# Kernel tuning notes

Measured on AMD Instinct MI355X. Metric: run time of the kernel, lower is better.

The kernel has to match this reference:

```python
import jax, jax.numpy as jnp
import numpy as np

B, S, K, N = 4, 2048, 4096, 4096

def setup_inputs() -> dict:
    key = jax.random.key(0)
    k1, k2, k3, k4 = jax.random.split(key, 4)
    # int8 quantized activations and weight (stored as int8, matmul accumulates int32)
    a = jax.random.randint(k1, (B, S, K), -128, 128, dtype=jnp.int32).astype(jnp.int8)
    w = jax.random.randint(k3, (K, N), -128, 128, dtype=jnp.int32).astype(jnp.int8)
    # dequant scales: per-token for activations, per-output-channel for weight
    a_s = (jax.random.uniform(k2, (B, S, 1), dtype=jnp.float32) + 0.5) * 0.01
    w_s = (jax.random.uniform(k4, (1, N), dtype=jnp.float32) + 0.5) * 0.01
    return {"a": a, "a_s": a_s, "w": w, "w_s": w_s}

def reference(a, a_s, w, w_s):
    # torch._int_mm loop with padding), fused with dequant epilogue.
    acc = jnp.einsum('bsk,kn->bsn', a, w, preferred_element_type=jnp.int32)
    # dequant: float32 accum * input_scale * weight_scale, cast to model dtype (fp16)
    out = (acc.astype(jnp.float32) * a_s * w_s).astype(jnp.float16)
    return out
```

## Files before the change

### kernel.cpp

```cpp
#include <hip/hip_runtime.h>
#include <cstdint>
#include <cstddef>


#define M_DIM 8192
#define N_DIM 4096
#define K_DIM 4096

#define PREP_A_BLOCKS ((M_DIM / 32) * (K_DIM / 128))
#define PREP_W_BLOCKS ((N_DIM / 64) * (K_DIM / 64))

typedef int v4i  __attribute__((ext_vector_type(4)));
typedef int v16i __attribute__((ext_vector_type(16)));

__device__ __forceinline__ uint32_t pack4(int x, int y, int z, int w)
{
    return (uint32_t)(x & 0xff) | ((uint32_t)(y & 0xff) << 8) |
           ((uint32_t)(z & 0xff) << 16) | ((uint32_t)(w & 0xff) << 24);
}

__global__ void __launch_bounds__(256) prepare_kernel(
    const int* __restrict__ a, const int* __restrict__ w,
    uint8_t* __restrict__ a_f, uint8_t* __restrict__ w_f)
{
    __shared__ int lds[64][65];
    const int t = threadIdx.x;

    if (blockIdx.x < PREP_A_BLOCKS) {
        uint32_t* l32 = (uint32_t*)&lds[0][0];
        const int bm = blockIdx.x >> 5;
        const int bk = blockIdx.x & 31;
        const int m0 = bm * 32;
        const int k0 = bk * 128;
#pragma unroll
        for (int i = 0; i < 4; ++i) {
            const int f = i * 256 + t;
            const int r = f >> 5;
            const int c = (f << 2) & 127;
            int4 x = *(const int4*)(a + (size_t)(m0 + r) * K_DIM + k0 + c);
            uint32_t u = pack4(x.x, x.y, x.z, x.w);
            const int region = c >> 5;
            const int chunk  = r + (((c >> 4) & 1) << 5);
            const int wd     = region * 256 + chunk * 4 + ((c & 15) >> 2);
            l32[wd ^ ((region & 3) << 3)] = u;
        }
        __syncthreads();
        uint4 o = ((const uint4*)l32)[t ^ (((t >> 6) & 3) << 1)];
        *(uint4*)(a_f + ((size_t)bm * 128 + bk * 4) * 1024 + t * 16) = o;
        return;
    }

    const int tile = blockIdx.x - PREP_A_BLOCKS;
    const int n0 = (tile & 63) * 64;
    const int k0 = (tile >> 6) * 64;

#pragma unroll
    for (int i = 0; i < 4; ++i) {
        int v   = t + 256 * i;
        int row = v >> 4;
        int cq  = v & 15;
        int4 x = *(const int4*)(w + (size_t)(k0 + row) * N_DIM + n0 + cq * 4);
        lds[row][cq * 4 + 0] = x.x;
        lds[row][cq * 4 + 1] = x.y;
        lds[row][cq * 4 + 2] = x.z;
        lds[row][cq * 4 + 3] = x.w;
    }
    __syncthreads();

    const int chunk  = t & 63;
    const int r_out  = t >> 6;
    const int nb     = r_out >> 1;
    const int kk     = r_out & 1;
    const int ncol   = nb * 32 + (chunk & 31);
    const int parity = chunk >> 5;
    const int rbase  = kk * 32 + parity * 16;
    uint32_t o[4];
#pragma unroll
    for (int q = 0; q < 4; ++q)
        o[q] = pack4(lds[rbase + q * 4 + 0][ncol],
                     lds[rbase + q * 4 + 1][ncol],
                     lds[rbase + q * 4 + 2][ncol],
                     lds[rbase + q * 4 + 3][ncol]);
    *(uint4*)(w_f + (((size_t)(n0 >> 5) + nb) * 128 + (k0 >> 5) + kk) * 1024
                  + chunk * 16) = make_uint4(o[0], o[1], o[2], o[3]);
}

__device__ __forceinline__ void async_copy16(const void* gptr, void* lptr)
{
    __builtin_amdgcn_global_load_lds(
        (const __attribute__((address_space(1))) uint32_t*)gptr,
        (__attribute__((address_space(3))) uint32_t*)lptr,
        16, 0, 0);
}

#define VMCNT4() asm volatile("s_waitcnt vmcnt(4)" ::: "memory")
#define VMCNT0() asm volatile("s_waitcnt vmcnt(0)" ::: "memory")

__global__ void __launch_bounds__(512, 2) int8_gemm_kernel(
    const uint8_t* __restrict__ Af,
    const uint8_t* __restrict__ Wf,
    const float*   __restrict__ a_s,
    const float*   __restrict__ w_s,
    float*         __restrict__ out)
{
    __shared__ __align__(16) uint8_t sA[2][4][8][1024];
    __shared__ __align__(16) uint8_t sB[2][4][8][1024];

    const int tid   = threadIdx.x;
    const int wave  = tid >> 6;
    const int lane  = tid & 63;
    const int waveM = wave >> 2;
    const int waveN = wave & 3;

    const int bid = blockIdx.x;
    const int xc  = bid & 7;
    const int j   = bid >> 3;
    const int bm  = (xc & 3) * 8 + (j & 7);
    const int bn  = (xc >> 2) * 8 + (j >> 3);
    const int m0  = bm * 256;
    const int n0  = bn * 256;

    v16i acc[4][2];
#pragma unroll
    for (int i = 0; i < 4; ++i)
#pragma unroll
        for (int jj = 0; jj < 2; ++jj)
#pragma unroll
            for (int r = 0; r < 16; ++r)
                acc[i][jj][r] = 0;

    const uint8_t* aBase = Af + (((size_t)(m0 >> 5) + wave) * 128) * 1024 + lane * 16;
    const uint8_t* bBase = Wf + (((size_t)(n0 >> 5) + wave) * 128) * 1024 + lane * 16;

    auto stage2 = [&](int buf, int kt, int s0) {
#pragma unroll
        for (int s = s0; s < s0 + 2; ++s) {
            async_copy16(aBase + (size_t)(kt * 4 + s) * 1024, &sA[buf][s][wave][0]);
            async_copy16(bBase + (size_t)(kt * 4 + s) * 1024, &sB[buf][s][wave][0]);
        }
    };

    auto compute_kstep = [&](int buf, int s) {
        v4i af[4], bf[2];
#pragma unroll
        for (int mt = 0; mt < 4; ++mt)
            af[mt] = *(const v4i*)(&sA[buf][s][waveM * 4 + mt][lane * 16]);
#pragma unroll
        for (int nt = 0; nt < 2; ++nt)
            bf[nt] = *(const v4i*)(&sB[buf][s][waveN * 2 + nt][lane * 16]);
        __builtin_amdgcn_s_setprio(1);
#pragma unroll
        for (int mt = 0; mt < 4; ++mt)
#pragma unroll
            for (int nt = 0; nt < 2; ++nt)
                acc[mt][nt] = __builtin_amdgcn_mfma_i32_32x32x32_i8(
                    af[mt], bf[nt], acc[mt][nt], 0, 0, 0);
        __builtin_amdgcn_s_setprio(0);
    };

    const int NT = K_DIM / 128;

    stage2(0, 0, 0);
    stage2(0, 0, 2);
    VMCNT4();
    __builtin_amdgcn_s_barrier();

    for (int kt = 0; kt < NT - 1; ++kt) {
        const int b = kt & 1;
        stage2(b ^ 1, kt + 1, 0);
        compute_kstep(b, 0);
        compute_kstep(b, 1);
        VMCNT4();
        __builtin_amdgcn_s_barrier();
        stage2(b ^ 1, kt + 1, 2);
        compute_kstep(b, 2);
        compute_kstep(b, 3);
        VMCNT4();
        __builtin_amdgcn_s_barrier();
    }
    {
        const int b = (NT - 1) & 1;
        compute_kstep(b, 0);
        compute_kstep(b, 1);
        VMCNT0();
        __builtin_amdgcn_s_barrier();
        compute_kstep(b, 2);
        compute_kstep(b, 3);
    }

    const int col   = lane & 31;
    const int rbase = (lane >> 5) * 4;

#pragma unroll
    for (int mt = 0; mt < 4; ++mt) {
        const int mrow0 = m0 + waveM * 128 + mt * 32 + rbase;
        float asv[16];
#pragma unroll
        for (int reg = 0; reg < 16; ++reg)
            asv[reg] = a_s[mrow0 + (reg & 3) + 8 * (reg >> 2)];
#pragma unroll
        for (int nt = 0; nt < 2; ++nt) {
            const int n = n0 + waveN * 64 + nt * 32 + col;
            const float wsv = w_s[n];
#pragma unroll
            for (int reg = 0; reg < 16; ++reg) {
                const int row = mrow0 + (reg & 3) + 8 * (reg >> 2);
                float v = (float)acc[mt][nt][reg] * asv[reg] * wsv;
                v = (float)(_Float16)v;
                out[(size_t)row * N_DIM + n] = v;
            }
        }
    }
}

extern "C" void kernel_launch(void* const* d_in, const int* in_sizes, int n_in,
                              void* d_out, int out_size, void* d_ws, size_t ws_size,
                              hipStream_t stream)
{
    const int*   a   = (const int*)  d_in[0];
    const float* a_s = (const float*)d_in[1];
    const int*   w   = (const int*)  d_in[2];
    const float* w_s = (const float*)d_in[3];
    float*       out = (float*)d_out;

    uint8_t* w_f = (uint8_t*)d_ws;
    uint8_t* a_f = (uint8_t*)d_ws + (size_t)N_DIM * K_DIM;

    prepare_kernel<<<PREP_A_BLOCKS + PREP_W_BLOCKS, 256, 0, stream>>>(
        a, w, a_f, w_f);

    int8_gemm_kernel<<<(M_DIM / 256) * (N_DIM / 256), 512, 0, stream>>>(
        a_f, w_f, a_s, w_s, out);
}
```

Before: 406.0 us.

## Restructure GEMM main loop into per-kstep fine-grained async copy pipeline

Replaces the two-half-per-tile staging with a per-k-step schedule. Each step reads its LDS fragments, issues the next tile's async global-to-LDS copy for that slot, passes a barrier, waits on lgkmcnt, runs the MFMAs, then waits on vmcnt(6) before another barrier. Sched barriers pin the instruction order. The goal is to spread global loads evenly and overlap them with MFMA work, at the cost of twice as many barriers per tile and tighter vmcnt accounting that could expose load latency.

```diff
diff --git a/kernel.cpp b/kernel.cpp
--- a/kernel.cpp
+++ b/kernel.cpp
@@ -93,8 +93,9 @@
         16, 0, 0);
 }
 
-#define VMCNT4() asm volatile("s_waitcnt vmcnt(4)" ::: "memory")
-#define VMCNT0() asm volatile("s_waitcnt vmcnt(0)" ::: "memory")
+#define WAIT_VMCNT(n) asm volatile("s_waitcnt vmcnt(" #n ")" ::: "memory")
+#define WAIT_LGKM0()  asm volatile("s_waitcnt lgkmcnt(0)" ::: "memory")
+#define SCHED_FENCE() __builtin_amdgcn_sched_barrier(0)
 
 __global__ void __launch_bounds__(512, 2) int8_gemm_kernel(
     const uint8_t* __restrict__ Af,
@@ -132,60 +133,79 @@
     const uint8_t* aBase = Af + (((size_t)(m0 >> 5) + wave) * 128) * 1024 + lane * 16;
     const uint8_t* bBase = Wf + (((size_t)(n0 >> 5) + wave) * 128) * 1024 + lane * 16;
 
-    auto stage2 = [&](int buf, int kt, int s0) {
-#pragma unroll
-        for (int s = s0; s < s0 + 2; ++s) {
-            async_copy16(aBase + (size_t)(kt * 4 + s) * 1024, &sA[buf][s][wave][0]);
-            async_copy16(bBase + (size_t)(kt * 4 + s) * 1024, &sB[buf][s][wave][0]);
-        }
-    };
-
-    auto compute_kstep = [&](int buf, int s) {
-        v4i af[4], bf[2];
-#pragma unroll
-        for (int mt = 0; mt < 4; ++mt)
-            af[mt] = *(const v4i*)(&sA[buf][s][waveM * 4 + mt][lane * 16]);
-#pragma unroll
-        for (int nt = 0; nt < 2; ++nt)
-            bf[nt] = *(const v4i*)(&sB[buf][s][waveN * 2 + nt][lane * 16]);
-        __builtin_amdgcn_s_setprio(1);
-#pragma unroll
-        for (int mt = 0; mt < 4; ++mt)
-#pragma unroll
-            for (int nt = 0; nt < 2; ++nt)
-                acc[mt][nt] = __builtin_amdgcn_mfma_i32_32x32x32_i8(
-                    af[mt], bf[nt], acc[mt][nt], 0, 0, 0);
-        __builtin_amdgcn_s_setprio(0);
-    };
-
     const int NT = K_DIM / 128;
 
-    stage2(0, 0, 0);
-    stage2(0, 0, 2);
-    VMCNT4();
+#pragma unroll
+    for (int s = 0; s < 4; ++s) {
+        async_copy16(aBase + (size_t)s * 1024, &sA[0][s][wave][0]);
+        async_copy16(bBase + (size_t)s * 1024, &sB[0][s][wave][0]);
+    }
+    WAIT_VMCNT(6);
+    SCHED_FENCE();
     __builtin_amdgcn_s_barrier();
 
     for (int kt = 0; kt < NT - 1; ++kt) {
         const int b = kt & 1;
-        stage2(b ^ 1, kt + 1, 0);
-        compute_kstep(b, 0);
-        compute_kstep(b, 1);
-        VMCNT4();
-        __builtin_amdgcn_s_barrier();
-        stage2(b ^ 1, kt + 1, 2);
-        compute_kstep(b, 2);
-        compute_kstep(b, 3);
-        VMCNT4();
-        __builtin_amdgcn_s_barrier();
-    }
+#pragma unroll
+        for (int s = 0; s < 4; ++s) {
+            v4i af[4], bf[2];
+#pragma unroll
+            for (int mt = 0; mt < 4; ++mt)
+                af[mt] = *(const v4i*)(&sA[b][s][waveM * 4 + mt][lane * 16]);
+#pragma unroll
+            for (int nt = 0; nt < 2; ++nt)
+                bf[nt] = *(const v4i*)(&sB[b][s][waveN * 2 + nt][lane * 16]);
+            async_copy16(aBase + (size_t)((kt + 1) * 4 + s) * 1024,
+                         &sA[b ^ 1][s][wave][0]);
+            async_copy16(bBase + (size_t)((kt + 1) * 4 + s) * 1024,
+                         &sB[b ^ 1][s][wave][0]);
+            SCHED_FENCE();
+            __builtin_amdgcn_s_barrier();
+            WAIT_LGKM0();
+            SCHED_FENCE();
+            __builtin_amdgcn_s_setprio(1);
+#pragma unroll
+            for (int mt = 0; mt < 4; ++mt)
+#pragma unroll
+                for (int nt = 0; nt < 2; ++nt)
+                    acc[mt][nt] = __builtin_amdgcn_mfma_i32_32x32x32_i8(
+                        af[mt], bf[nt], acc[mt][nt], 0, 0, 0);
+            __builtin_amdgcn_s_setprio(0);
+            WAIT_VMCNT(6);
+            SCHED_FENCE();
+            __builtin_amdgcn_s_barrier();
+        }
+    }
+
     {
         const int b = (NT - 1) & 1;
-        compute_kstep(b, 0);
-        compute_kstep(b, 1);
-        VMCNT0();
-        __builtin_amdgcn_s_barrier();
-        compute_kstep(b, 2);
-        compute_kstep(b, 3);
+#pragma unroll
+        for (int s = 0; s < 4; ++s) {
+            v4i af[4], bf[2];
+#pragma unroll
+            for (int mt = 0; mt < 4; ++mt)
+                af[mt] = *(const v4i*)(&sA[b][s][waveM * 4 + mt][lane * 16]);
+#pragma unroll
+            for (int nt = 0; nt < 2; ++nt)
+                bf[nt] = *(const v4i*)(&sB[b][s][waveN * 2 + nt][lane * 16]);
+            SCHED_FENCE();
+            __builtin_amdgcn_s_barrier();
+            WAIT_LGKM0();
+            SCHED_FENCE();
+            __builtin_amdgcn_s_setprio(1);
+#pragma unroll
+            for (int mt = 0; mt < 4; ++mt)
+#pragma unroll
+                for (int nt = 0; nt < 2; ++nt)
+                    acc[mt][nt] = __builtin_amdgcn_mfma_i32_32x32x32_i8(
+                        af[mt], bf[nt], acc[mt][nt], 0, 0, 0);
+            __builtin_amdgcn_s_setprio(0);
+            if (s == 0) { WAIT_VMCNT(4); }
+            else if (s == 1) { WAIT_VMCNT(2); }
+            else if (s == 2) { WAIT_VMCNT(0); }
+            SCHED_FENCE();
+            if (s < 3) __builtin_amdgcn_s_barrier();
+        }
     }
 
     const int col   = lane & 31;
```

New measurement: 394.4 us. 2.9% less time.

## Software-pipeline LDS fragment reads against MFMAs with register double-buffering

Applied to the files above, without the earlier changes.

Splits each k-step into LDS fragment reads and MFMA issue, and prefetches the next k-step's fragments into a second register set while the current MFMAs run, with scheduling fences to keep that order. Global-to-LDS copies are issued one A/B pair per k-step, and the two partial waits per tile become a single full vmcnt(0) wait and barrier. The aim is to hide LDS read latency behind matrix-core work. The cost is more live vector registers under a 2-waves-per-SIMD bound, and a full memory drain at every tile boundary.

```diff
diff --git a/kernel.cpp b/kernel.cpp
--- a/kernel.cpp
+++ b/kernel.cpp
@@ -93,8 +93,8 @@
         16, 0, 0);
 }
 
-#define VMCNT4() asm volatile("s_waitcnt vmcnt(4)" ::: "memory")
-#define VMCNT0() asm volatile("s_waitcnt vmcnt(0)" ::: "memory")
+#define WAIT_VMCNT0() asm volatile("s_waitcnt vmcnt(0)" ::: "memory")
+#define SCHED_FENCE() __builtin_amdgcn_sched_barrier(0)
 
 __global__ void __launch_bounds__(512, 2) int8_gemm_kernel(
     const uint8_t* __restrict__ Af,
@@ -132,22 +132,21 @@
     const uint8_t* aBase = Af + (((size_t)(m0 >> 5) + wave) * 128) * 1024 + lane * 16;
     const uint8_t* bBase = Wf + (((size_t)(n0 >> 5) + wave) * 128) * 1024 + lane * 16;
 
-    auto stage2 = [&](int buf, int kt, int s0) {
-#pragma unroll
-        for (int s = s0; s < s0 + 2; ++s) {
-            async_copy16(aBase + (size_t)(kt * 4 + s) * 1024, &sA[buf][s][wave][0]);
-            async_copy16(bBase + (size_t)(kt * 4 + s) * 1024, &sB[buf][s][wave][0]);
-        }
+    auto stage_pair = [&](int buf, int kt, int s) {
+        async_copy16(aBase + (size_t)(kt * 4 + s) * 1024, &sA[buf][s][wave][0]);
+        async_copy16(bBase + (size_t)(kt * 4 + s) * 1024, &sB[buf][s][wave][0]);
     };
 
-    auto compute_kstep = [&](int buf, int s) {
-        v4i af[4], bf[2];
+    auto ds_read6 = [&](v4i (&af)[4], v4i (&bf)[2], int buf, int s) {
 #pragma unroll
         for (int mt = 0; mt < 4; ++mt)
             af[mt] = *(const v4i*)(&sA[buf][s][waveM * 4 + mt][lane * 16]);
 #pragma unroll
         for (int nt = 0; nt < 2; ++nt)
             bf[nt] = *(const v4i*)(&sB[buf][s][waveN * 2 + nt][lane * 16]);
+    };
+
+    auto mfma8 = [&](v4i (&af)[4], v4i (&bf)[2]) {
         __builtin_amdgcn_s_setprio(1);
 #pragma unroll
         for (int mt = 0; mt < 4; ++mt)
@@ -160,32 +159,58 @@
 
     const int NT = K_DIM / 128;
 
-    stage2(0, 0, 0);
-    stage2(0, 0, 2);
-    VMCNT4();
+    v4i afA[4], bfA[2], afB[4], bfB[2];
+
+#pragma unroll
+    for (int s = 0; s < 4; ++s)
+        stage_pair(0, 0, s);
+    WAIT_VMCNT0();
+    SCHED_FENCE();
     __builtin_amdgcn_s_barrier();
+    ds_read6(afA, bfA, 0, 0);
 
     for (int kt = 0; kt < NT - 1; ++kt) {
         const int b = kt & 1;
-        stage2(b ^ 1, kt + 1, 0);
-        compute_kstep(b, 0);
-        compute_kstep(b, 1);
-        VMCNT4();
+        stage_pair(b ^ 1, kt + 1, 0);
+        ds_read6(afB, bfB, b, 1);
+        SCHED_FENCE();
+        mfma8(afA, bfA);
+        SCHED_FENCE();
+        stage_pair(b ^ 1, kt + 1, 1);
+        ds_read6(afA, bfA, b, 2);
+        SCHED_FENCE();
+        mfma8(afB, bfB);
+        SCHED_FENCE();
+        stage_pair(b ^ 1, kt + 1, 2);
+        ds_read6(afB, bfB, b, 3);
+        SCHED_FENCE();
+        mfma8(afA, bfA);
+        SCHED_FENCE();
+        stage_pair(b ^ 1, kt + 1, 3);
+        SCHED_FENCE();
+        mfma8(afB, bfB);
+        SCHED_FENCE();
+        WAIT_VMCNT0();
+        SCHED_FENCE();
         __builtin_amdgcn_s_barrier();
-        stage2(b ^ 1, kt + 1, 2);
-        compute_kstep(b, 2);
-        compute_kstep(b, 3);
-        VMCNT4();
-        __builtin_amdgcn_s_barrier();
-    }
+        ds_read6(afA, bfA, b ^ 1, 0);
+    }
+
     {
         const int b = (NT - 1) & 1;
-        compute_kstep(b, 0);
-        compute_kstep(b, 1);
-        VMCNT0();
-        __builtin_amdgcn_s_barrier();
-        compute_kstep(b, 2);
-        compute_kstep(b, 3);
+        ds_read6(afB, bfB, b, 1);
+        SCHED_FENCE();
+        mfma8(afA, bfA);
+        SCHED_FENCE();
+        ds_read6(afA, bfA, b, 2);
+        SCHED_FENCE();
+        mfma8(afB, bfB);
+        SCHED_FENCE();
+        ds_read6(afB, bfB, b, 3);
+        SCHED_FENCE();
+        mfma8(afA, bfA);
+        SCHED_FENCE();
+        mfma8(afB, bfB);
     }
 
     const int col   = lane & 31;
```

Result: no change. 409.1 us (+0.8%).
